# Optimization experiments

Hardware: AMD Instinct MI355X
Metric: run time of the kernel (lower is better)

Reference implementation:

```python
import jax, jax.numpy as jnp
import numpy as np
from jax import lax

B, N, K, NUM_CLASS = 8, 4096, 16, 13


def knn(pc, k):
    # pc: (B, C, N); returns indices of k nearest neighbors (B, N, k)
    sq = jnp.sum(pc * pc, axis=1)                       # (B, N)
    inner = jnp.einsum('bcn,bcm->bnm', pc, pc)          # (B, N, N)
    neg_dist = 2.0 * inner - sq[:, :, None] - sq[:, None, :]
    return lax.top_k(neg_dist, k)[1]                    # (B, N, k)


def group(fea, idx):
    # fea: (B, C, N), idx: (B, N, k) -> (B, C, N, k)
    return jax.vmap(lambda f, i: f[:, i])(fea, idx)


def mlp2(x, w, b, act=True):
    # 1x1 conv2d: x (B, Cin, N, k) -> (B, Cout, N, k)
    y = jnp.einsum('oc,bcnk->bonk', w, x) + b[None, :, None, None]
    return jax.nn.relu(y) if act else y


def mlp1(x, w, b, act=True):
    # 1x1 conv1d: x (B, Cin, N) -> (B, Cout, N)
    y = jnp.einsum('oc,bcn->bon', w, x) + b[None, :, None]
    return jax.nn.relu(y) if act else y


def edgeconv(xyz, fea, k, wg1, bg1, wg2, bg2, wf1, bf1, wf2, bf2, wf3, bf3):
    idx = knn(fea, k)
    # geometric branch: (B, 10, N, k) = [dist, xyz, xyz_knn, xyz - xyz_knn]
    xk = group(xyz, idx)
    xc = jnp.broadcast_to(xyz[:, :, :, None], xk.shape)
    xr = xc - xk
    xd = jnp.sqrt(jnp.sum(xr * xr, axis=1, keepdims=True))
    g = jnp.concatenate([xd, xc, xk, xr], axis=1)
    # feature branch: (B, 2C, N, k) = [fea, fea_knn]
    fk = group(fea, idx)
    fc = jnp.broadcast_to(fea[:, :, :, None], fk.shape)
    f = jnp.concatenate([fc, fk], axis=1)
    g = mlp2(mlp2(g, wg1, bg1), wg2, bg2)
    f = mlp2(mlp2(mlp2(f, wf1, bf1), wf2, bf2), wf3, bf3)
    return jnp.max(g * f, axis=-1)  # (B, Cout, N)


_SPECS = [
    ('e1_mg1', 10, 32), ('e1_mg2', 32, 32),
    ('e1_mf1', 6, 32), ('e1_mf2', 32, 32), ('e1_mf3', 32, 32),
    ('e2_mg1', 10, 128), ('e2_mg2', 128, 128),
    ('e2_mf1', 64, 128), ('e2_mf2', 128, 128), ('e2_mf3', 128, 128),
    ('c1', 128, 128), ('c2', 128, 1024), ('c3', 1184, 512),
    ('c4', 512, 256), ('c5', 256, 128), ('c6', 128, NUM_CLASS),
]


def setup_inputs() -> dict:
    key = jax.random.key(0)
    ks = jax.random.split(key, 2 * len(_SPECS) + 1)
    inp = {'xyz': jax.random.normal(ks[0], (B, N, 3), dtype=jnp.float32)}
    for j, (name, ci, co) in enumerate(_SPECS):
        scale = 1.0 / np.sqrt(ci)
        inp['w_' + name] = jax.random.normal(ks[2 * j + 1], (co, ci), dtype=jnp.float32) * scale
        inp['b_' + name] = jax.random.normal(ks[2 * j + 2], (co,), dtype=jnp.float32) * 0.01
    return inp


def reference(xyz, w_e1_mg1, b_e1_mg1, w_e1_mg2, b_e1_mg2, w_e1_mf1, b_e1_mf1,
              w_e1_mf2, b_e1_mf2, w_e1_mf3, b_e1_mf3, w_e2_mg1, b_e2_mg1,
              w_e2_mg2, b_e2_mg2, w_e2_mf1, b_e2_mf1, w_e2_mf2, b_e2_mf2,
              w_e2_mf3, b_e2_mf3, w_c1, b_c1, w_c2, b_c2, w_c3, b_c3,
              w_c4, b_c4, w_c5, b_c5, w_c6, b_c6):
    x = jnp.transpose(xyz, (0, 2, 1))  # (B, 3, N)
    fea1 = edgeconv(x, x, K, w_e1_mg1, b_e1_mg1, w_e1_mg2, b_e1_mg2,
                    w_e1_mf1, b_e1_mf1, w_e1_mf2, b_e1_mf2, w_e1_mf3, b_e1_mf3)
    fea2 = edgeconv(x, fea1, K, w_e2_mg1, b_e2_mg1, w_e2_mg2, b_e2_mg2,
                    w_e2_mf1, b_e2_mf1, w_e2_mf2, b_e2_mf2, w_e2_mf3, b_e2_mf3)
    f = mlp1(fea2, w_c1, b_c1)
    f = mlp1(f, w_c2, b_c2)                        # (B, 1024, N)
    g = jnp.max(f, axis=-1, keepdims=True)         # global feature (B, 1024, 1)
    g = jnp.broadcast_to(g, (g.shape[0], g.shape[1], x.shape[2]))
    f = jnp.concatenate([fea1, fea2, g], axis=1)   # (B, 1184, N)
    f = mlp1(f, w_c3, b_c3)
    f = mlp1(f, w_c4, b_c4)
    f = mlp1(f, w_c5, b_c5)
    return mlp1(f, w_c6, b_c6, act=False)          # (B, NUM_CLASS, N)
```

## Files before the change

kernel.cpp:

```cpp
#include <hip/hip_runtime.h>
#include <math.h>

#define B_ 8
#define N_ 4096

__device__ __forceinline__ unsigned short bf16rne(float x) {
    unsigned int u = __float_as_uint(x);
    return (unsigned short)((u + 0x7FFFu + ((u >> 16) & 1u)) >> 16);
}
__device__ __forceinline__ float bff(unsigned short h) {
    return __uint_as_float((unsigned int)h << 16);
}
__device__ __forceinline__ void cvt_hl(unsigned short* base, int numel, int idx, float x) {
    unsigned short h = bf16rne(x);
    base[idx] = h;
    base[numel + idx] = bf16rne(x - bff(h));
}

typedef __attribute__((ext_vector_type(8))) short bf16x8;
typedef __attribute__((ext_vector_type(4))) float f32x4;

__global__ __launch_bounds__(256) void prep_kernel(
    const float* __restrict__ w0, const float* __restrict__ w1,
    const float* __restrict__ w2, const float* __restrict__ w3,
    const float* __restrict__ w4, const float* __restrict__ w5,
    const float* __restrict__ w6, const float* __restrict__ w8,
    const float* __restrict__ w9, const float* __restrict__ w10,
    const float* __restrict__ w11, const float* __restrict__ w12,
    const float* __restrict__ w13, const float* __restrict__ w14,
    const float* __restrict__ wf1, const float* __restrict__ bf1,
    const float* __restrict__ xyz,
    float* __restrict__ wt, float* __restrict__ gbuf, float* __restrict__ sqbuf) {
    const int g = blockIdx.x * 256 + threadIdx.x;
    unsigned short* wus = (unsigned short*)(wt + 3840);

    if (g < 3584) {
        if (g < 320)       { int i = g >> 5, o = g & 31;             wt[g] = w0[o * 10 + i]; }
        else if (g < 1344) { int l = g - 320;  int i = l >> 5, o = l & 31; wt[g] = w1[o * 32 + i]; }
        else if (g < 1536) { int l = g - 1344; int i = l >> 5, o = l & 31; wt[g] = w2[o * 6 + i]; }
        else if (g < 2560) { int l = g - 1536; int i = l >> 5, o = l & 31; wt[g] = w3[o * 32 + i]; }
        else               { int l = g - 2560; int i = l >> 5, o = l & 31; wt[g] = w4[o * 32 + i]; }
    }
    else if (g < 3840)   { int l = g - 3584; wt[g] = (l < 128) ? bf1[l] : 0.0f; }
    else if (g < 12032)  { int l = g - 3840; int o = l >> 5, i = l & 31;
                           float x = (o < 128) ? wf1[o * 64 + i] : wf1[(o - 128) * 64 + 32 + i];
                           cvt_hl(wus + 0, 8192, l, x); }
    else if (g < 28416)  { int l = g - 12032;  cvt_hl(wus + 16384, 16384, l, w10[l]); }
    else if (g < 159488) { int l = g - 28416;  cvt_hl(wus + 49152, 131072, l, w11[l]); }
    else if (g < 241408) { int l = g - 159488; int o = l / 160, i = l - o * 160;
                           cvt_hl(wus + 311296, 81920, l, w12[o * 1184 + i]); }
    else if (g < 372480) { int l = g - 241408; cvt_hl(wus + 475136, 131072, l, w13[l]); }
    else if (g < 405248) { int l = g - 372480; cvt_hl(wus + 737280, 32768, l, w14[l]); }
    else if (g < 409344) { int l = g - 405248; int o = l >> 5, k = l & 31;
                           float x = (k < 10) ? w5[o * 10 + k] : 0.0f;
                           cvt_hl(wus + 802816, 4096, l, x); }
    else if (g < 425728) { int l = g - 409344; cvt_hl(wus + 811008, 16384, l, w6[l]); }
    else if (g < 442112) { int l = g - 425728; cvt_hl(wus + 843776, 16384, l, w8[l]); }
    else if (g < 458496) { int l = g - 442112; cvt_hl(wus + 876544, 16384, l, w9[l]); }
    else if (g < 466688) { gbuf[g - 458496] = 0.0f; }
    else if (g < 499456) { int l = g - 466688;
                           const float* p = xyz + (size_t)l * 3;
                           sqbuf[l] = fmaf(p[0], p[0], fmaf(p[1], p[1], p[2] * p[2])); }
}

template<int C>
__global__ void sq_kernel(const float* __restrict__ F, float* __restrict__ SQ) {
    int idx = blockIdx.x * 256 + threadIdx.x;
    const float* p = F + (size_t)idx * C;
    float s = 0.0f;
    #pragma unroll
    for (int c = 0; c < C; ++c) s = fmaf(p[c], p[c], s);
    SQ[idx] = s;
}


__device__ __forceinline__ void cas_asc(unsigned long long& x, unsigned long long& y) {
    unsigned long long a = x, b = y;
    bool sw = a > b;
    x = sw ? b : a;
    y = sw ? a : b;
}

__device__ __forceinline__ void merge_top(unsigned long long (&k)[16],
                                          const unsigned long long (&o)[16]) {
    #pragma unroll
    for (int i = 0; i < 16; ++i) {
        unsigned long long bb = o[15 - i];
        if (bb > k[i]) k[i] = bb;
    }
    #pragma unroll
    for (int st = 8; st >= 1; st >>= 1)
        #pragma unroll
        for (int i = 0; i < 16; ++i)
            if ((i & st) == 0) cas_asc(k[i], k[i + st]);
}

__device__ __forceinline__ void casf(float& x, float& y, int& xi, int& yi) {
    bool sw = x > y;
    float a = sw ? y : x;  float b = sw ? x : y;
    int ai = sw ? yi : xi; int bi = sw ? xi : yi;
    x = a; y = b; xi = ai; yi = bi;
}

__device__ __forceinline__ void sort16f(float (&v)[16], int (&ix)[16]) {
    #pragma unroll
    for (int sz = 2; sz <= 16; sz <<= 1)
        #pragma unroll
        for (int st = sz >> 1; st >= 1; st >>= 1)
            #pragma unroll
            for (int i = 0; i < 16; ++i)
                if ((i & st) == 0) {
                    if ((i & sz) == 0) casf(v[i], v[i + st], ix[i], ix[i + st]);
                    else                casf(v[i + st], v[i], ix[i + st], ix[i]);
                }
}

__device__ __forceinline__ void merge_topf(float (&kv)[16], int (&ki)[16],
                                           const float (&nv)[16], const int (&ni)[16]) {
    #pragma unroll
    for (int i = 0; i < 16; ++i) {
        bool tk = nv[15 - i] > kv[i];
        kv[i] = tk ? nv[15 - i] : kv[i];
        ki[i] = tk ? ni[15 - i] : ki[i];
    }
    #pragma unroll
    for (int st = 8; st >= 1; st >>= 1)
        #pragma unroll
        for (int i = 0; i < 16; ++i)
            if ((i & st) == 0) casf(kv[i], kv[i + st], ki[i], ki[i + st]);
}

template<int C>
__global__ __launch_bounds__(256, 3) void knn_kernel(
    const float* __restrict__ F, const float* __restrict__ SQ,
    unsigned long long* __restrict__ Kout) {
    constexpr int P1F = 2 * C * 68 + 64 * 72;
    constexpr int P1W = (P1F + 1) / 2;
    constexpr int SMW = (P1W > 64 * 65) ? P1W : 64 * 65;
    __shared__ __align__(16) unsigned long long SM[SMW];
    __shared__ float sqr[64];
    __shared__ float sqc[64];
    float* Rf = (float*)SM;
    float* Cf = Rf + C * 68;
    float* Ds = Cf + C * 68;
    const int t = threadIdx.x;
    const int b = blockIdx.y;
    const int r0 = blockIdx.x * 64;
    const int half = blockIdx.z;
    const int H0 = half * 2048;
    const int rt = (t & 15) * 4, ct = (t >> 4) * 4;
    const int sr = t & 63, sq = t >> 6;

    for (int idx = t; idx < 64 * C; idx += 256) {
        int rr = idx / C, c = idx - rr * C;
        Rf[c * 68 + rr] = F[((size_t)b * N_ + r0 + rr) * C + c];
    }
    if (t < 64) sqr[t] = SQ[(size_t)b * N_ + r0 + t];

    float kv[16]; int ki[16];
    #pragma unroll
    for (int j = 0; j < 16; ++j) { kv[j] = -3.4e38f; ki[j] = 0; }

    for (int c0 = H0; c0 < H0 + 2048; c0 += 64) {
        for (int idx = t; idx < 64 * C; idx += 256) {
            int cc = idx / C, c = idx - cc * C;
            Cf[c * 68 + cc] = F[((size_t)b * N_ + c0 + cc) * C + c];
        }
        if (t < 64) sqc[t] = SQ[(size_t)b * N_ + c0 + t];
        __syncthreads();

        float acc[4][4];
        #pragma unroll
        for (int ii = 0; ii < 4; ++ii)
            #pragma unroll
            for (int jj = 0; jj < 4; ++jj) acc[ii][jj] = 0.0f;
        #pragma unroll
        for (int i = 0; i < C; ++i) {
            float a4[4], w4[4];
            *(float4*)a4 = *(const float4*)&Rf[i * 68 + rt];
            *(float4*)w4 = *(const float4*)&Cf[i * 68 + ct];
            #pragma unroll
            for (int ii = 0; ii < 4; ++ii)
                #pragma unroll
                for (int jj = 0; jj < 4; ++jj)
                    acc[ii][jj] = fmaf(a4[ii], w4[jj], acc[ii][jj]);
        }
        #pragma unroll
        for (int ii = 0; ii < 4; ++ii) {
            float e[4];
            #pragma unroll
            for (int jj = 0; jj < 4; ++jj)
                e[jj] = 2.0f * acc[ii][jj] - sqr[rt + ii] - sqc[ct + jj];
            *(float2*)&Ds[(rt + ii) * 72 + ct] = make_float2(e[0], e[1]);
            *(float2*)&Ds[(rt + ii) * 72 + ct + 2] = make_float2(e[2], e[3]);
        }
        __syncthreads();

        float nv[16]; int ni[16];
        *(float4*)&nv[0]  = *(const float4*)&Ds[sr * 72 + sq * 16 + 0];
        *(float4*)&nv[4]  = *(const float4*)&Ds[sr * 72 + sq * 16 + 4];
        *(float4*)&nv[8]  = *(const float4*)&Ds[sr * 72 + sq * 16 + 8];
        *(float4*)&nv[12] = *(const float4*)&Ds[sr * 72 + sq * 16 + 12];
        #pragma unroll
        for (int s = 0; s < 16; ++s) ni[s] = c0 + sq * 16 + s;
        sort16f(nv, ni);
        merge_topf(kv, ki, nv, ni);
    }
    __syncthreads();
    unsigned long long kl[16];
    #pragma unroll
    for (int j = 0; j < 16; ++j) {
        unsigned int u = __float_as_uint(kv[j]);
        unsigned int ou = (u & 0x80000000u) ? ~u : (u | 0x80000000u);
        kl[j] = ((unsigned long long)ou << 32) | (unsigned int)(4095 - ki[j]);
    }
    unsigned long long* QL = SM;
    #pragma unroll
    for (int j = 0; j < 16; ++j) QL[sr * 65 + sq * 16 + j] = kl[j];
    __syncthreads();
    if (t < 64) {
        unsigned long long K[16], Tt[16];
        #pragma unroll
        for (int j = 0; j < 16; ++j) K[j] = QL[t * 65 + j];
        #pragma unroll
        for (int q = 1; q < 4; ++q) {
            #pragma unroll
            for (int j = 0; j < 16; ++j) Tt[j] = QL[t * 65 + q * 16 + j];
            merge_top(K, Tt);
        }
        size_t obase = (((size_t)b * 2 + half) * N_ + r0 + t) * 16;
        #pragma unroll
        for (int j = 0; j < 16; ++j) Kout[obase + j] = K[j];
    }
}

__global__ __launch_bounds__(256) void knn_merge_kernel(
    const unsigned long long* __restrict__ Kbuf, int* __restrict__ IDX) {
    int gid = blockIdx.x * 256 + threadIdx.x;
    int b = gid >> 12, r = gid & 4095;
    unsigned long long K0[16], K1[16];
    const unsigned long long* p0 = Kbuf + (((size_t)b * 2 + 0) * N_ + r) * 16;
    const unsigned long long* p1 = Kbuf + (((size_t)b * 2 + 1) * N_ + r) * 16;
    #pragma unroll
    for (int j = 0; j < 16; ++j) { K0[j] = p0[j]; K1[j] = p1[j]; }
    merge_top(K0, K1);
    size_t ob = ((size_t)b * N_ + r) * 16;
    #pragma unroll
    for (int j = 0; j < 16; ++j)
        IDX[ob + j] = 4095 - (int)(unsigned int)(K0[15 - j] & 0xFFFFFFFFu);
}


__global__ __launch_bounds__(256, 4) void e1_kernel(
    const float* __restrict__ xyz, const int* __restrict__ idx1,
    const float* __restrict__ wte1,
    const float* __restrict__ bg1, const float* __restrict__ bg2,
    const float* __restrict__ bf1, const float* __restrict__ bf2,
    const float* __restrict__ bf3,
    float* __restrict__ fea1) {
    __shared__ __align__(16) float Ain[10 * 132];
    __shared__ __align__(16) float Bu0[32 * 132];
    __shared__ __align__(16) float Bu1[32 * 132];
    __shared__ __align__(16) float wl[3584];
    __shared__ float bl[5][32];
    __shared__ __align__(16) float Pm1[4][8][32];
    __shared__ int idxl[128];
    const int t = threadIdx.x;
    const int b = blockIdx.x >> 9;
    const int n0 = (blockIdx.x & 511) << 3;
    const int et = (t & 31) << 2;
    const int ct = (t >> 5) << 2;

    for (int i = t; i < 3584; i += 256) wl[i] = wte1[i];
    if (t < 32) {
        bl[0][t] = bg1[t]; bl[1][t] = bg2[t]; bl[2][t] = bf1[t];
        bl[3][t] = bf2[t]; bl[4][t] = bf3[t];
    }
    if (t < 128) idxl[t] = idx1[((size_t)b * N_ + n0 + (t >> 4)) * 16 + (t & 15)];
    __syncthreads();
    if (t < 128) {
        int p = t >> 4, n = n0 + p, m = idxl[t];
        const float* xc = xyz + ((size_t)b * N_ + n) * 3;
        const float* xk = xyz + ((size_t)b * N_ + m) * 3;
        float c0 = xc[0], c1v = xc[1], c2v = xc[2];
        float k0 = xk[0], k1 = xk[1], k2 = xk[2];
        float r0 = c0 - k0, r1 = c1v - k1, r2 = c2v - k2;
        Ain[0 * 132 + t] = sqrtf(r0 * r0 + r1 * r1 + r2 * r2);
        Ain[1 * 132 + t] = c0;  Ain[2 * 132 + t] = c1v; Ain[3 * 132 + t] = c2v;
        Ain[4 * 132 + t] = k0;  Ain[5 * 132 + t] = k1;  Ain[6 * 132 + t] = k2;
        Ain[7 * 132 + t] = r0;  Ain[8 * 132 + t] = r1;  Ain[9 * 132 + t] = r2;
    }
    __syncthreads();

    float acc[4][4];
    auto gem = [&](int KK, const float* Asrc, int woff) {
        #pragma unroll
        for (int ii = 0; ii < 4; ++ii)
            #pragma unroll
            for (int jj = 0; jj < 4; ++jj) acc[ii][jj] = 0.0f;
        for (int i = 0; i < KK; ++i) {
            float a4[4], w4[4];
            *(float4*)a4 = *(const float4*)&Asrc[i * 132 + et];
            *(float4*)w4 = *(const float4*)&wl[woff + i * 32 + ct];
            #pragma unroll
            for (int ii = 0; ii < 4; ++ii)
                #pragma unroll
                for (int jj = 0; jj < 4; ++jj)
                    acc[ii][jj] = fmaf(a4[ii], w4[jj], acc[ii][jj]);
        }
    };
    auto wrout = [&](float* dst, const float* brow) {
        #pragma unroll
        for (int jj = 0; jj < 4; ++jj) {
            float tmp[4];
            #pragma unroll
            for (int ii = 0; ii < 4; ++ii) tmp[ii] = fmaxf(acc[ii][jj] + brow[ct + jj], 0.0f);
            *(float4*)&dst[(ct + jj) * 132 + et] = *(float4*)tmp;
        }
    };

    gem(10, Ain, 0);          wrout(Bu1, bl[0]);   __syncthreads();
    gem(32, Bu1, 320);
    float g2r[4][4];
    #pragma unroll
    for (int ii = 0; ii < 4; ++ii)
        #pragma unroll
        for (int jj = 0; jj < 4; ++jj)
            g2r[ii][jj] = fmaxf(acc[ii][jj] + bl[1][ct + jj], 0.0f);
    gem(6, Ain + 132, 1344);  wrout(Bu0, bl[2]);   __syncthreads();
    gem(32, Bu0, 1536);       wrout(Bu1, bl[3]);   __syncthreads();
    gem(32, Bu1, 2560);

    float pm[4];
    #pragma unroll
    for (int jj = 0; jj < 4; ++jj) {
        float mx = 0.0f;
        #pragma unroll
        for (int ii = 0; ii < 4; ++ii) {
            float f3 = fmaxf(acc[ii][jj] + bl[4][ct + jj], 0.0f);
            mx = fmaxf(mx, g2r[ii][jj] * f3);
        }
        pm[jj] = mx;
    }
    const int sub = t & 3, pl = (t & 31) >> 2;
    *(float4*)&Pm1[sub][pl][ct] = *(float4*)pm;
    __syncthreads();
    {
        int p = t >> 5, c = t & 31;
        float v = fmaxf(fmaxf(Pm1[0][p][c], Pm1[1][p][c]), fmaxf(Pm1[2][p][c], Pm1[3][p][c]));
        fea1[((size_t)b * N_ + n0 + p) * 32 + c] = v;
    }
}


__global__ __launch_bounds__(256, 2) void e2_kernel(
    const float* __restrict__ xyz, const int* __restrict__ idx2,
    const float* __restrict__ CfPf,
    const unsigned short* __restrict__ wg1p, const unsigned short* __restrict__ wg2p,
    const unsigned short* __restrict__ wf2p, const unsigned short* __restrict__ wf3p,
    const float* __restrict__ bg1, const float* __restrict__ bg2,
    const float* __restrict__ bf2, const float* __restrict__ bf3,
    float* __restrict__ fea2) {
    __shared__ __align__(16) unsigned short Ah[128 * 128];
    __shared__ __align__(16) unsigned short Al[128 * 128];
    __shared__ float bb[4][128];
    __shared__ int idxl[128];
    const int t = threadIdx.x;
    const int b = blockIdx.x >> 9;
    const int n0 = (blockIdx.x & 511) << 3;
    const int lane = t & 63, w = t >> 6;
    const int wr = (w >> 1) << 6;
    const int wc = (w & 1) << 6;
    const int lr = lane & 15, lg = lane >> 4;
    const int kb = lg << 3;

    auto swz = [](int e, int bo) { return e * 256 + (bo ^ ((e & 7) << 4)); };

    for (int i = t; i < 512; i += 256) {
        const float* bp = (i < 128) ? bg1 : (i < 256) ? bg2 : (i < 384) ? bf2 : bf3;
        bb[i >> 7][i & 127] = bp[i & 127];
    }
    if (t < 128) idxl[t] = idx2[((size_t)b * N_ + n0 + (t >> 4)) * 16 + (t & 15)];
    __syncthreads();

    f32x4 acc[4][4];
    const f32x4 zz = {0.0f, 0.0f, 0.0f, 0.0f};
    auto zacc = [&]() {
        #pragma unroll
        for (int i = 0; i < 4; ++i)
            #pragma unroll
            for (int j = 0; j < 4; ++j) acc[i][j] = zz;
    };

    {
        bf16x8 gbh[4], gbl[4];
        #pragma unroll
        for (int j = 0; j < 4; ++j) {
            float gv[8];
            #pragma unroll
            for (int q = 0; q < 8; ++q) gv[q] = 0.0f;
            if (lg < 2) {
                int e = wc + j * 16 + lr;
                int p = e >> 4, m = idxl[e];
                const float* xc = xyz + ((size_t)b * N_ + n0 + p) * 3;
                const float* xk = xyz + ((size_t)b * N_ + m) * 3;
                float c0 = xc[0], c1 = xc[1], c2 = xc[2];
                float k0 = xk[0], k1 = xk[1], k2 = xk[2];
                float r0 = c0 - k0, r1 = c1 - k1, r2 = c2 - k2;
                if (lg == 0) {
                    gv[0] = sqrtf(r0 * r0 + r1 * r1 + r2 * r2);
                    gv[1] = c0; gv[2] = c1; gv[3] = c2;
                    gv[4] = k0; gv[5] = k1; gv[6] = k2; gv[7] = r0;
                } else { gv[0] = r1; gv[1] = r2; }
            }
            bf16x8 vh, vl;
            #pragma unroll
            for (int q = 0; q < 8; ++q) {
                unsigned short h = bf16rne(gv[q]);
                vh[q] = (short)h;
                vl[q] = (short)bf16rne(gv[q] - bff(h));
            }
            gbh[j] = vh; gbl[j] = vl;
        }
        zacc();
        #pragma unroll
        for (int i = 0; i < 4; ++i) {
            size_t off = (size_t)(wr + i * 16 + lr) * 32 + kb;
            bf16x8 wh = *(const bf16x8*)(wg1p + off);
            bf16x8 wl_ = *(const bf16x8*)(wg1p + 4096 + off);
            #pragma unroll
            for (int j = 0; j < 4; ++j) {
                acc[i][j] = __builtin_amdgcn_mfma_f32_16x16x32_bf16(wh, gbh[j], acc[i][j], 0, 0, 0);
                acc[i][j] = __builtin_amdgcn_mfma_f32_16x16x32_bf16(wl_, gbh[j], acc[i][j], 0, 0, 0);
                acc[i][j] = __builtin_amdgcn_mfma_f32_16x16x32_bf16(wh, gbl[j], acc[i][j], 0, 0, 0);
            }
        }
    }

    auto epi_store = [&](const float* brow) {
        #pragma unroll
        for (int i = 0; i < 4; ++i) {
            int o4 = wr + i * 16 + lg * 4;
            float bv[4];
            *(float4*)bv = *(const float4*)&brow[o4];
            #pragma unroll
            for (int j = 0; j < 4; ++j) {
                int e = wc + j * 16 + lr;
                unsigned short h[4], l[4];
                #pragma unroll
                for (int r = 0; r < 4; ++r) {
                    float v = fmaxf(acc[i][j][r] + bv[r], 0.0f);
                    h[r] = bf16rne(v);
                    l[r] = bf16rne(v - bff(h[r]));
                }
                int bo = swz(e, o4 * 2);
                *(ushort4*)((char*)Ah + bo) = make_ushort4(h[0], h[1], h[2], h[3]);
                *(ushort4*)((char*)Al + bo) = make_ushort4(l[0], l[1], l[2], l[3]);
            }
        }
    };
    epi_store(bb[0]);
    __syncthreads();

    auto gemmK = [&](const unsigned short* __restrict__ Wp) {
        zacc();
        #pragma unroll
        for (int ks = 0; ks < 4; ++ks) {
            bf16x8 xh[4], xl[4];
            #pragma unroll
            for (int j = 0; j < 4; ++j) {
                int e = wc + j * 16 + lr;
                int bo = swz(e, (ks * 32 + kb) * 2);
                xh[j] = *(const bf16x8*)((const char*)Ah + bo);
                xl[j] = *(const bf16x8*)((const char*)Al + bo);
            }
            #pragma unroll
            for (int i = 0; i < 4; ++i) {
                size_t off = (size_t)(wr + i * 16 + lr) * 128 + ks * 32 + kb;
                bf16x8 wh = *(const bf16x8*)(Wp + off);
                bf16x8 wl_ = *(const bf16x8*)(Wp + 16384 + off);
                #pragma unroll
                for (int j = 0; j < 4; ++j) {
                    acc[i][j] = __builtin_amdgcn_mfma_f32_16x16x32_bf16(wh, xh[j], acc[i][j], 0, 0, 0);
                    acc[i][j] = __builtin_amdgcn_mfma_f32_16x16x32_bf16(wl_, xh[j], acc[i][j], 0, 0, 0);
                    acc[i][j] = __builtin_amdgcn_mfma_f32_16x16x32_bf16(wh, xl[j], acc[i][j], 0, 0, 0);
                }
            }
        }
    };

    gemmK(wg2p);
    float g2r[4][4][4];
    #pragma unroll
    for (int i = 0; i < 4; ++i) {
        float bv[4];
        *(float4*)bv = *(const float4*)&bb[1][wr + i * 16 + lg * 4];
        #pragma unroll
        for (int j = 0; j < 4; ++j)
            #pragma unroll
            for (int r = 0; r < 4; ++r)
                g2r[i][j][r] = fmaxf(acc[i][j][r] + bv[r], 0.0f);
    }
    __syncthreads();

    {
        int e = t & 127, hf = t >> 7;
        int n = n0 + (e >> 4), m = idxl[e];
        const float* crow = CfPf + ((size_t)b * N_ + n) * 256 + hf * 64;
        const float* prow = CfPf + ((size_t)b * N_ + m) * 256 + 128 + hf * 64;
        #pragma unroll
        for (int q = 0; q < 16; ++q) {
            float4 cc = *(const float4*)(crow + q * 4);
            float4 pp = *(const float4*)(prow + q * 4);
            float v[4] = { fmaxf(cc.x + pp.x, 0.0f), fmaxf(cc.y + pp.y, 0.0f),
                           fmaxf(cc.z + pp.z, 0.0f), fmaxf(cc.w + pp.w, 0.0f) };
            unsigned short h[4], l[4];
            #pragma unroll
            for (int r = 0; r < 4; ++r) {
                h[r] = bf16rne(v[r]);
                l[r] = bf16rne(v[r] - bff(h[r]));
            }
            int bo = swz(e, (hf * 64 + q * 4) * 2);
            *(ushort4*)((char*)Ah + bo) = make_ushort4(h[0], h[1], h[2], h[3]);
            *(ushort4*)((char*)Al + bo) = make_ushort4(l[0], l[1], l[2], l[3]);
        }
    }
    __syncthreads();

    gemmK(wf2p);
    __syncthreads();
    epi_store(bb[2]);
    __syncthreads();

    gemmK(wf3p);
    #pragma unroll
    for (int j = 0; j < 4; ++j) {
        int p = (wc >> 4) + j;
        #pragma unroll
        for (int i = 0; i < 4; ++i) {
            int o4 = wr + i * 16 + lg * 4;
            float bv[4];
            *(float4*)bv = *(const float4*)&bb[3][o4];
            float vr[4];
            #pragma unroll
            for (int r = 0; r < 4; ++r) {
                float f3v = fmaxf(acc[i][j][r] + bv[r], 0.0f);
                float v = g2r[i][j][r] * f3v;
                v = fmaxf(v, __shfl_xor(v, 1));
                v = fmaxf(v, __shfl_xor(v, 2));
                v = fmaxf(v, __shfl_xor(v, 4));
                v = fmaxf(v, __shfl_xor(v, 8));
                vr[r] = v;
            }
            if (lr == 0)
                *(float4*)(fea2 + ((size_t)b * N_ + n0 + p) * 128 + o4) = *(float4*)vr;
        }
    }
}


template<int RELU, int BMODE, int GMAX>
__global__ __launch_bounds__(256) void gemm_mfma(
    const float* __restrict__ X1, int S1, int K1,
    const float* __restrict__ X2, int S2, int Ktot,
    const unsigned short* __restrict__ Wc, const float* __restrict__ bias,
    float* __restrict__ Y, int COUT, float* __restrict__ gout) {
    __shared__ __align__(16) unsigned short Xh[128 * 40];
    __shared__ __align__(16) unsigned short Xl[128 * 40];
    __shared__ __align__(16) unsigned short Wh[128 * 40];
    __shared__ __align__(16) unsigned short Wl[128 * 40];
    __shared__ float Gm[2][128];
    const int t = threadIdx.x;
    const int m0 = blockIdx.x * 128, o0 = blockIdx.y * 128;
    const int lane = t & 63, w = t >> 6;
    const int wr = (w >> 1) << 6, wc = (w & 1) << 6;
    const int lr = lane & 15, lg = lane >> 4;
    const int kb = lg << 3;
    const size_t WN = (size_t)COUT * Ktot;

    f32x4 acc[4][4];
    const f32x4 zz = {0.0f, 0.0f, 0.0f, 0.0f};
    #pragma unroll
    for (int i = 0; i < 4; ++i)
        #pragma unroll
        for (int j = 0; j < 4; ++j) acc[i][j] = zz;

    const int ntile = Ktot >> 5;
    for (int kt = 0; kt < ntile; ++kt) {
        const int kbase = kt << 5;
        const float* Xp; int S, koff;
        if (kbase < K1) { Xp = X1; S = S1; koff = kbase; }
        else            { Xp = X2; S = S2; koff = kbase - K1; }
        #pragma unroll
        for (int rr = 0; rr < 4; ++rr) {
            int idx = t + rr * 256;
            int p = idx >> 3, i4 = (idx & 7) << 2;
            const float4 v = *(const float4*)(Xp + (size_t)(m0 + p) * S + koff + i4);
            unsigned short h0 = bf16rne(v.x), h1 = bf16rne(v.y);
            unsigned short h2 = bf16rne(v.z), h3 = bf16rne(v.w);
            *(ushort4*)&Xh[p * 40 + i4] = make_ushort4(h0, h1, h2, h3);
            *(ushort4*)&Xl[p * 40 + i4] = make_ushort4(
                bf16rne(v.x - bff(h0)), bf16rne(v.y - bff(h1)),
                bf16rne(v.z - bff(h2)), bf16rne(v.w - bff(h3)));
        }
        #pragma unroll
        for (int rr = 0; rr < 2; ++rr) {
            int c = t + rr * 256;
            int o = c >> 2, k8 = (c & 3) << 3;
            const unsigned short* src = Wc + (size_t)(o0 + o) * Ktot + kbase + k8;
            *(uint4*)&Wh[o * 40 + k8] = *(const uint4*)src;
            *(uint4*)&Wl[o * 40 + k8] = *(const uint4*)(src + WN);
        }
        __syncthreads();

        bf16x8 ah[4], al[4], bh[4], bl[4];
        #pragma unroll
        for (int f = 0; f < 4; ++f) {
            ah[f] = *(const bf16x8*)&Xh[(wr + f * 16 + lr) * 40 + kb];
            al[f] = *(const bf16x8*)&Xl[(wr + f * 16 + lr) * 40 + kb];
            bh[f] = *(const bf16x8*)&Wh[(wc + f * 16 + lr) * 40 + kb];
            bl[f] = *(const bf16x8*)&Wl[(wc + f * 16 + lr) * 40 + kb];
        }
        #pragma unroll
        for (int i = 0; i < 4; ++i)
            #pragma unroll
            for (int j = 0; j < 4; ++j) {
                acc[i][j] = __builtin_amdgcn_mfma_f32_16x16x32_bf16(ah[i], bh[j], acc[i][j], 0, 0, 0);
                acc[i][j] = __builtin_amdgcn_mfma_f32_16x16x32_bf16(al[i], bh[j], acc[i][j], 0, 0, 0);
                acc[i][j] = __builtin_amdgcn_mfma_f32_16x16x32_bf16(ah[i], bl[j], acc[i][j], 0, 0, 0);
            }
        __syncthreads();
    }

    const int b = m0 >> 12;
    if (GMAX) {
        #pragma unroll
        for (int j = 0; j < 4; ++j) {
            const int oc = wc + j * 16 + lr;
            const float bv = bias[o0 + oc];
            float mx = 0.0f;
            #pragma unroll
            for (int i = 0; i < 4; ++i)
                #pragma unroll
                for (int r = 0; r < 4; ++r) {
                    float v = acc[i][j][r] + bv;
                    if (RELU) v = fmaxf(v, 0.0f);
                    mx = fmaxf(mx, v);
                }
            mx = fmaxf(mx, __shfl_xor(mx, 16));
            mx = fmaxf(mx, __shfl_xor(mx, 32));
            if (lane < 16) Gm[w >> 1][wc + j * 16 + lane] = mx;
        }
        __syncthreads();
        if (t < 128) {
            float v = fmaxf(Gm[0][t], Gm[1][t]);
            atomicMax((unsigned int*)(gout + b * 1024 + o0 + t), __float_as_uint(v));
        }
    } else {
        #pragma unroll
        for (int j = 0; j < 4; ++j) {
            const int oc = wc + j * 16 + lr;
            const float bv = (BMODE == 0) ? bias[o0 + oc] : bias[b * 512 + o0 + oc];
            #pragma unroll
            for (int i = 0; i < 4; ++i) {
                float* yp = Y + (size_t)(m0 + wr + i * 16 + lg * 4) * COUT + o0 + oc;
                #pragma unroll
                for (int r = 0; r < 4; ++r) {
                    float v = acc[i][j][r] + bv;
                    if (RELU) v = fmaxf(v, 0.0f);
                    yp[(size_t)r * COUT] = v;
                }
            }
        }
    }
}


__global__ void bias3_kernel(const float* __restrict__ g, const float* __restrict__ w_c3,
                             const float* __restrict__ b_c3, float* __restrict__ bias3) {
    __shared__ float gs[1024];
    int b = blockIdx.x >> 1;
    int o = ((blockIdx.x & 1) << 8) + threadIdx.x;
    for (int i = threadIdx.x; i < 1024; i += 256) gs[i] = g[b * 1024 + i];
    __syncthreads();
    float acc = b_c3[o];
    const float* wr = w_c3 + (size_t)o * 1184 + 160;
    for (int i = 0; i < 1024; i += 4) {
        float4 w4 = *(const float4*)(wr + i);
        acc = fmaf(w4.x, gs[i], acc);     acc = fmaf(w4.y, gs[i + 1], acc);
        acc = fmaf(w4.z, gs[i + 2], acc); acc = fmaf(w4.w, gs[i + 3], acc);
    }
    bias3[b * 512 + o] = acc;
}


__global__ __launch_bounds__(256, 1) void c6_kernel(
    const float* __restrict__ h5, const float* __restrict__ w,
    const float* __restrict__ bias, float* __restrict__ out) {
    __shared__ float ws[13 * 128];
    __shared__ float bs[13];
    int t = threadIdx.x;
    for (int i = t; i < 13 * 128; i += 256) ws[i] = w[i];
    if (t < 13) bs[t] = bias[t];
    __syncthreads();
    int b = blockIdx.x >> 4;
    int n = ((blockIdx.x & 15) << 8) + t;
    float x[128];
    const float* xp = h5 + ((size_t)b * N_ + n) * 128;
    #pragma unroll
    for (int i = 0; i < 128; i += 4) *(float4*)&x[i] = *(const float4*)(xp + i);
    for (int o = 0; o < 13; ++o) {
        float acc = bs[o];
        #pragma unroll
        for (int i = 0; i < 128; ++i) acc = fmaf(ws[o * 128 + i], x[i], acc);
        out[((size_t)b * 13 + o) * N_ + n] = acc;
    }
}


extern "C" void kernel_launch(void* const* d_in, const int* in_sizes, int n_in,
                              void* d_out, int out_size, void* d_ws, size_t ws_size,
                              hipStream_t stream) {
    (void)in_sizes; (void)n_in; (void)out_size; (void)ws_size;
    const float* xyz = (const float*)d_in[0];
    #define W_(j)  ((const float*)d_in[1 + 2 * (j)])
    #define Bp_(j) ((const float*)d_in[2 + 2 * (j)])

    char* ws = (char*)d_ws;
    const size_t MB = 1u << 20;
    int*   idx1  = (int*)(ws + 0 * MB);
    int*   idx2  = (int*)(ws + 2 * MB);
    float* fea1  = (float*)(ws + 4 * MB);
    float* CfPf  = (float*)(ws + 8 * MB);
    float* fea2  = (float*)(ws + 40 * MB);
    float* h1    = (float*)(ws + 56 * MB);
    float* sqbuf = (float*)(ws + 72 * MB);
    float* gbuf  = (float*)(ws + 72 * MB + (128u << 10));
    float* b3buf = (float*)(ws + 72 * MB + (160u << 10));
    float* wt    = (float*)(ws + 72 * MB + (176u << 10));
    float* h3    = (float*)(ws + 75 * MB);
    float* h4    = CfPf;
    float* h5    = h1;
    float* outp  = (float*)d_out;
    unsigned long long* Kbuf = (unsigned long long*)(ws + 75 * MB);

    float* wte1  = wt;
    float* bpre  = wt + 3584;
    const unsigned short* wus = (const unsigned short*)(wt + 3840);
    const unsigned short* wpre = wus + 0;
    const unsigned short* wc1  = wus + 16384;
    const unsigned short* wc2  = wus + 49152;
    const unsigned short* wc3  = wus + 311296;
    const unsigned short* wc4  = wus + 475136;
    const unsigned short* wc5  = wus + 737280;
    const unsigned short* wg1p = wus + 802816;
    const unsigned short* wg2p = wus + 811008;
    const unsigned short* wf2p = wus + 843776;
    const unsigned short* wf3p = wus + 876544;

    prep_kernel<<<1951, 256, 0, stream>>>(
        W_(0), W_(1), W_(2), W_(3), W_(4), W_(5), W_(6), W_(8), W_(9), W_(10),
        W_(11), W_(12), W_(13), W_(14), W_(7), Bp_(7), xyz, wt, gbuf, sqbuf);

    knn_kernel<3><<<dim3(64, 8, 2), 256, 0, stream>>>(xyz, sqbuf, Kbuf);
    knn_merge_kernel<<<128, 256, 0, stream>>>(Kbuf, idx1);
    e1_kernel<<<4096, 256, 0, stream>>>(xyz, idx1, wte1, Bp_(0), Bp_(1), Bp_(2), Bp_(3), Bp_(4), fea1);

    sq_kernel<32><<<128, 256, 0, stream>>>(fea1, sqbuf);
    knn_kernel<32><<<dim3(64, 8, 2), 256, 0, stream>>>(fea1, sqbuf, Kbuf);
    knn_merge_kernel<<<128, 256, 0, stream>>>(Kbuf, idx2);
    gemm_mfma<0, 0, 0><<<dim3(256, 2), 256, 0, stream>>>(fea1, 32, 32, nullptr, 0, 32,
                                                         wpre, bpre, CfPf, 256, nullptr);
    e2_kernel<<<4096, 256, 0, stream>>>(xyz, idx2, CfPf, wg1p, wg2p, wf2p, wf3p,
                                        Bp_(5), Bp_(6), Bp_(8), Bp_(9), fea2);

    gemm_mfma<1, 0, 0><<<dim3(256, 1), 256, 0, stream>>>(fea2, 128, 128, nullptr, 0, 128,
                                                         wc1, Bp_(10), h1, 128, nullptr);
    gemm_mfma<1, 0, 1><<<dim3(256, 8), 256, 0, stream>>>(h1, 128, 128, nullptr, 0, 128,
                                                         wc2, Bp_(11), nullptr, 1024, gbuf);
    bias3_kernel<<<16, 256, 0, stream>>>(gbuf, W_(12), Bp_(12), b3buf);
    gemm_mfma<1, 1, 0><<<dim3(256, 4), 256, 0, stream>>>(fea1, 32, 32, fea2, 128, 160,
                                                         wc3, b3buf, h3, 512, nullptr);
    gemm_mfma<1, 0, 0><<<dim3(256, 2), 256, 0, stream>>>(h3, 512, 512, nullptr, 0, 512,
                                                         wc4, Bp_(13), h4, 256, nullptr);
    gemm_mfma<1, 0, 0><<<dim3(256, 1), 256, 0, stream>>>(h4, 256, 256, nullptr, 0, 256,
                                                         wc5, Bp_(14), h5, 128, nullptr);
    c6_kernel<<<128, 256, 0, stream>>>(h5, W_(15), Bp_(15), outp);
    #undef W_
    #undef Bp_
}
```

Measured before the change: 1.216 ms.

## Move KNN distance computation to bf16x3 MFMA with two-pass threshold selection

The KNN kernel now computes the pairwise inner products on MFMA units, using a three-way bf16 split (high/mid/low) of the features that prep_kernel and a new fea1p_kernel pack ahead of time. It runs two passes: the first keeps only the sorted top-16 values per row to derive a threshold, and the second recomputes distances and collects candidates at or above that threshold into shared memory via atomics, then sorts them with their indices. This avoids carrying index arrays through the bitonic sorts and removes the fp32 FMA inner loop, at the cost of doing the MFMA work twice and reading operands directly from global memory. Candidate capture is capped at 32 per row, so ties could drop entries, and the split-bf16 product may not match fp32 bit-for-bit.

```diff
diff --git a/kernel.cpp b/kernel.cpp
--- a/kernel.cpp
+++ b/kernel.cpp
@@ -3,6 +3,7 @@
 
 #define B_ 8
 #define N_ 4096
+#define PL_ (8 * 4096 * 32)
 
 __device__ __forceinline__ unsigned short bf16rne(float x) {
     unsigned int u = __float_as_uint(x);
@@ -19,6 +20,8 @@
 
 typedef __attribute__((ext_vector_type(8))) short bf16x8;
 typedef __attribute__((ext_vector_type(4))) float f32x4;
+
+#define MF16(a, b, c) __builtin_amdgcn_mfma_f32_16x16x32_bf16((a), (b), (c), 0, 0, 0)
 
 __global__ __launch_bounds__(256) void prep_kernel(
     const float* __restrict__ w0, const float* __restrict__ w1,
@@ -30,7 +33,8 @@
     const float* __restrict__ w13, const float* __restrict__ w14,
     const float* __restrict__ wf1, const float* __restrict__ bf1,
     const float* __restrict__ xyz,
-    float* __restrict__ wt, float* __restrict__ gbuf, float* __restrict__ sqbuf) {
+    float* __restrict__ wt, float* __restrict__ gbuf, float* __restrict__ sqbuf,
+    unsigned short* __restrict__ xyzp) {
     const int g = blockIdx.x * 256 + threadIdx.x;
     unsigned short* wus = (unsigned short*)(wt + 3840);
 
@@ -61,16 +65,51 @@
     else if (g < 499456) { int l = g - 466688;
                            const float* p = xyz + (size_t)l * 3;
                            sqbuf[l] = fmaf(p[0], p[0], fmaf(p[1], p[1], p[2] * p[2])); }
-}
-
-template<int C>
-__global__ void sq_kernel(const float* __restrict__ F, float* __restrict__ SQ) {
-    int idx = blockIdx.x * 256 + threadIdx.x;
-    const float* p = F + (size_t)idx * C;
+    else if (g < 532224) {
+        int row = g - 499456;
+        const float* p = xyz + (size_t)row * 3;
+        unsigned short hv[8] = {0,0,0,0,0,0,0,0};
+        unsigned short mv[8] = {0,0,0,0,0,0,0,0};
+        unsigned short lv[8] = {0,0,0,0,0,0,0,0};
+        #pragma unroll
+        for (int c = 0; c < 3; ++c) {
+            float v = p[c];
+            unsigned short h = bf16rne(v); float d = v - bff(h);
+            unsigned short m = bf16rne(d);
+            hv[c] = h; mv[c] = m; lv[c] = bf16rne(d - bff(m));
+        }
+        uint4 z = make_uint4(0u, 0u, 0u, 0u);
+        unsigned short* d0 = xyzp + (size_t)row * 32;
+        unsigned short* d1 = d0 + PL_;
+        unsigned short* d2 = d0 + 2 * PL_;
+        *(uint4*)d0 = *(uint4*)hv; *(uint4*)(d0 + 8) = z; *(uint4*)(d0 + 16) = z; *(uint4*)(d0 + 24) = z;
+        *(uint4*)d1 = *(uint4*)mv; *(uint4*)(d1 + 8) = z; *(uint4*)(d1 + 16) = z; *(uint4*)(d1 + 24) = z;
+        *(uint4*)d2 = *(uint4*)lv; *(uint4*)(d2 + 8) = z; *(uint4*)(d2 + 16) = z; *(uint4*)(d2 + 24) = z;
+    }
+}
+
+__global__ __launch_bounds__(256) void fea1p_kernel(
+    const float* __restrict__ F, unsigned short* __restrict__ P, float* __restrict__ SQ) {
+    int row = blockIdx.x * 256 + threadIdx.x;
+    const float* x = F + (size_t)row * 32;
     float s = 0.0f;
-    #pragma unroll
-    for (int c = 0; c < C; ++c) s = fmaf(p[c], p[c], s);
-    SQ[idx] = s;
+    unsigned short hb[32], mb[32], lb[32];
+    #pragma unroll
+    for (int c = 0; c < 32; ++c) {
+        float v = x[c];
+        s = fmaf(v, v, s);
+        unsigned short h = bf16rne(v); float d = v - bff(h);
+        unsigned short m = bf16rne(d);
+        hb[c] = h; mb[c] = m; lb[c] = bf16rne(d - bff(m));
+    }
+    SQ[row] = s;
+    unsigned short* d0 = P + (size_t)row * 32;
+    #pragma unroll
+    for (int q = 0; q < 4; ++q) {
+        *(uint4*)(d0 + 8 * q)           = *(uint4*)&hb[8 * q];
+        *(uint4*)(d0 + PL_ + 8 * q)     = *(uint4*)&mb[8 * q];
+        *(uint4*)(d0 + 2 * PL_ + 8 * q) = *(uint4*)&lb[8 * q];
+    }
 }
 
 
@@ -95,14 +134,12 @@
             if ((i & st) == 0) cas_asc(k[i], k[i + st]);
 }
 
-__device__ __forceinline__ void casf(float& x, float& y, int& xi, int& yi) {
-    bool sw = x > y;
-    float a = sw ? y : x;  float b = sw ? x : y;
-    int ai = sw ? yi : xi; int bi = sw ? xi : yi;
-    x = a; y = b; xi = ai; yi = bi;
-}
-
-__device__ __forceinline__ void sort16f(float (&v)[16], int (&ix)[16]) {
+__device__ __forceinline__ void casv(float& x, float& y) {
+    float lo = fminf(x, y), hi = fmaxf(x, y);
+    x = lo; y = hi;
+}
+
+__device__ __forceinline__ void sortv16(float (&v)[16]) {
     #pragma unroll
     for (int sz = 2; sz <= 16; sz <<= 1)
         #pragma unroll
@@ -110,123 +147,151 @@
             #pragma unroll
             for (int i = 0; i < 16; ++i)
                 if ((i & st) == 0) {
-                    if ((i & sz) == 0) casf(v[i], v[i + st], ix[i], ix[i + st]);
-                    else                casf(v[i + st], v[i], ix[i + st], ix[i]);
+                    if ((i & sz) == 0) casv(v[i], v[i + st]);
+                    else                casv(v[i + st], v[i]);
                 }
 }
 
-__device__ __forceinline__ void merge_topf(float (&kv)[16], int (&ki)[16],
-                                           const float (&nv)[16], const int (&ni)[16]) {
-    #pragma unroll
-    for (int i = 0; i < 16; ++i) {
-        bool tk = nv[15 - i] > kv[i];
-        kv[i] = tk ? nv[15 - i] : kv[i];
-        ki[i] = tk ? ni[15 - i] : ki[i];
-    }
+__device__ __forceinline__ void mergev(float (&kv)[16], const float (&nv)[16]) {
+    #pragma unroll
+    for (int i = 0; i < 16; ++i) kv[i] = fmaxf(kv[i], nv[15 - i]);
     #pragma unroll
     for (int st = 8; st >= 1; st >>= 1)
         #pragma unroll
         for (int i = 0; i < 16; ++i)
-            if ((i & st) == 0) casf(kv[i], kv[i + st], ki[i], ki[i + st]);
-}
-
-template<int C>
-__global__ __launch_bounds__(256, 3) void knn_kernel(
-    const float* __restrict__ F, const float* __restrict__ SQ,
+            if ((i & st) == 0) casv(kv[i], kv[i + st]);
+}
+
+__global__ __launch_bounds__(256, 4) void knn_kernel(
+    const unsigned short* __restrict__ P, const float* __restrict__ SQ,
     unsigned long long* __restrict__ Kout) {
-    constexpr int P1F = 2 * C * 68 + 64 * 72;
-    constexpr int P1W = (P1F + 1) / 2;
-    constexpr int SMW = (P1W > 64 * 65) ? P1W : 64 * 65;
-    __shared__ __align__(16) unsigned long long SM[SMW];
-    __shared__ float sqr[64];
-    __shared__ float sqc[64];
-    float* Rf = (float*)SM;
-    float* Cf = Rf + C * 68;
-    float* Ds = Cf + C * 68;
+    __shared__ __align__(16) char U[64 * 68 * 4];
+    __shared__ float sqcL[2048];
+    __shared__ float tau[64];
+    __shared__ int cnt[64];
+    float* Ds = (float*)U;
+    unsigned long long* cap = (unsigned long long*)U;
     const int t = threadIdx.x;
     const int b = blockIdx.y;
     const int r0 = blockIdx.x * 64;
     const int half = blockIdx.z;
     const int H0 = half * 2048;
-    const int rt = (t & 15) * 4, ct = (t >> 4) * 4;
+    const int lane = t & 63, w = t >> 6;
+    const int lr = lane & 15, lg = lane >> 4;
+    const int kb = lg << 3;
     const int sr = t & 63, sq = t >> 6;
-
-    for (int idx = t; idx < 64 * C; idx += 256) {
-        int rr = idx / C, c = idx - rr * C;
-        Rf[c * 68 + rr] = F[((size_t)b * N_ + r0 + rr) * C + c];
-    }
-    if (t < 64) sqr[t] = SQ[(size_t)b * N_ + r0 + t];
-
-    float kv[16]; int ki[16];
-    #pragma unroll
-    for (int j = 0; j < 16; ++j) { kv[j] = -3.4e38f; ki[j] = 0; }
+    const int pw = lg ^ (w & 3);
+    const int psr = ((sr >> 2) ^ (sr >> 4)) & 3;
+
+    for (int i = t; i < 2048; i += 256) sqcL[i] = SQ[(size_t)b * N_ + H0 + i];
+
+    const unsigned short* ap = P + ((size_t)(b * N_) + r0 + 16 * w + lr) * 32 + kb;
+    const bf16x8 ah = *(const bf16x8*)ap;
+    const bf16x8 am = *(const bf16x8*)(ap + PL_);
+    const bf16x8 al = *(const bf16x8*)(ap + 2 * PL_);
+    const f32x4 sqr4 = *(const f32x4*)&SQ[(size_t)b * N_ + r0 + 16 * w + 4 * lg];
+
+    float kv[16];
+    #pragma unroll
+    for (int j = 0; j < 16; ++j) kv[j] = -3.4e38f;
+
+    __syncthreads();
 
     for (int c0 = H0; c0 < H0 + 2048; c0 += 64) {
-        for (int idx = t; idx < 64 * C; idx += 256) {
-            int cc = idx / C, c = idx - cc * C;
-            Cf[c * 68 + cc] = F[((size_t)b * N_ + c0 + cc) * C + c];
-        }
-        if (t < 64) sqc[t] = SQ[(size_t)b * N_ + c0 + t];
+        #pragma unroll
+        for (int j = 0; j < 4; ++j) {
+            const unsigned short* bp = P + ((size_t)(b * N_) + c0 + 16 * j + lr) * 32 + kb;
+            bf16x8 bh = *(const bf16x8*)bp;
+            bf16x8 bm = *(const bf16x8*)(bp + PL_);
+            bf16x8 bl = *(const bf16x8*)(bp + 2 * PL_);
+            f32x4 a = {0.0f, 0.0f, 0.0f, 0.0f};
+            a = MF16(ah, bh, a); a = MF16(am, bh, a); a = MF16(ah, bm, a);
+            a = MF16(am, bm, a); a = MF16(al, bh, a); a = MF16(ah, bl, a);
+            float sqcv = sqcL[c0 - H0 + 16 * j + lr];
+            int colsw = 16 * j + ((((lr >> 2) ^ pw) & 3) << 2) + (lr & 3);
+            #pragma unroll
+            for (int r = 0; r < 4; ++r) {
+                float e = fmaf(2.0f, a[r], -sqr4[r]) - sqcv;
+                Ds[(16 * w + 4 * lg + r) * 68 + colsw] = e;
+            }
+        }
         __syncthreads();
-
-        float acc[4][4];
-        #pragma unroll
-        for (int ii = 0; ii < 4; ++ii)
-            #pragma unroll
-            for (int jj = 0; jj < 4; ++jj) acc[ii][jj] = 0.0f;
-        #pragma unroll
-        for (int i = 0; i < C; ++i) {
-            float a4[4], w4[4];
-            *(float4*)a4 = *(const float4*)&Rf[i * 68 + rt];
-            *(float4*)w4 = *(const float4*)&Cf[i * 68 + ct];
-            #pragma unroll
-            for (int ii = 0; ii < 4; ++ii)
+        float nv[16];
+        #pragma unroll
+        for (int q = 0; q < 4; ++q)
+            *(float4*)&nv[4 * q] = *(const float4*)&Ds[sr * 68 + sq * 16 + (((q ^ psr) & 3) << 2)];
+        sortv16(nv);
+        mergev(kv, nv);
+        __syncthreads();
+    }
+
+    float* QLf = (float*)U;
+    #pragma unroll
+    for (int j = 0; j < 16; ++j) QLf[sr * 68 + sq * 16 + j] = kv[j];
+    __syncthreads();
+    if (t < 64) {
+        float K[16];
+        #pragma unroll
+        for (int j = 0; j < 16; ++j) K[j] = QLf[t * 68 + j];
+        #pragma unroll
+        for (int q = 1; q < 4; ++q) {
+            float Tt[16];
+            #pragma unroll
+            for (int j = 0; j < 16; ++j) Tt[j] = QLf[t * 68 + q * 16 + j];
+            #pragma unroll
+            for (int i = 0; i < 16; ++i) K[i] = fmaxf(K[i], Tt[15 - i]);
+            #pragma unroll
+            for (int st = 8; st >= 1; st >>= 1)
                 #pragma unroll
-                for (int jj = 0; jj < 4; ++jj)
-                    acc[ii][jj] = fmaf(a4[ii], w4[jj], acc[ii][jj]);
-        }
-        #pragma unroll
-        for (int ii = 0; ii < 4; ++ii) {
-            float e[4];
-            #pragma unroll
-            for (int jj = 0; jj < 4; ++jj)
-                e[jj] = 2.0f * acc[ii][jj] - sqr[rt + ii] - sqc[ct + jj];
-            *(float2*)&Ds[(rt + ii) * 72 + ct] = make_float2(e[0], e[1]);
-            *(float2*)&Ds[(rt + ii) * 72 + ct + 2] = make_float2(e[2], e[3]);
-        }
-        __syncthreads();
-
-        float nv[16]; int ni[16];
-        *(float4*)&nv[0]  = *(const float4*)&Ds[sr * 72 + sq * 16 + 0];
-        *(float4*)&nv[4]  = *(const float4*)&Ds[sr * 72 + sq * 16 + 4];
-        *(float4*)&nv[8]  = *(const float4*)&Ds[sr * 72 + sq * 16 + 8];
-        *(float4*)&nv[12] = *(const float4*)&Ds[sr * 72 + sq * 16 + 12];
-        #pragma unroll
-        for (int s = 0; s < 16; ++s) ni[s] = c0 + sq * 16 + s;
-        sort16f(nv, ni);
-        merge_topf(kv, ki, nv, ni);
-    }
-    __syncthreads();
-    unsigned long long kl[16];
-    #pragma unroll
-    for (int j = 0; j < 16; ++j) {
-        unsigned int u = __float_as_uint(kv[j]);
-        unsigned int ou = (u & 0x80000000u) ? ~u : (u | 0x80000000u);
-        kl[j] = ((unsigned long long)ou << 32) | (unsigned int)(4095 - ki[j]);
-    }
-    unsigned long long* QL = SM;
-    #pragma unroll
-    for (int j = 0; j < 16; ++j) QL[sr * 65 + sq * 16 + j] = kl[j];
-    __syncthreads();
+                for (int i = 0; i < 16; ++i)
+                    if ((i & st) == 0) casv(K[i], K[i + st]);
+        }
+        tau[t] = K[0];
+        cnt[t] = 0;
+    }
+    __syncthreads();
+    const f32x4 taur4 = *(const f32x4*)&tau[16 * w + 4 * lg];
+
+    for (int c0 = H0; c0 < H0 + 2048; c0 += 64) {
+        #pragma unroll
+        for (int j = 0; j < 4; ++j) {
+            const unsigned short* bp = P + ((size_t)(b * N_) + c0 + 16 * j + lr) * 32 + kb;
+            bf16x8 bh = *(const bf16x8*)bp;
+            bf16x8 bm = *(const bf16x8*)(bp + PL_);
+            bf16x8 bl = *(const bf16x8*)(bp + 2 * PL_);
+            f32x4 a = {0.0f, 0.0f, 0.0f, 0.0f};
+            a = MF16(ah, bh, a); a = MF16(am, bh, a); a = MF16(ah, bm, a);
+            a = MF16(am, bm, a); a = MF16(al, bh, a); a = MF16(ah, bl, a);
+            float sqcv = sqcL[c0 - H0 + 16 * j + lr];
+            #pragma unroll
+            for (int r = 0; r < 4; ++r) {
+                float e = fmaf(2.0f, a[r], -sqr4[r]) - sqcv;
+                if (e >= taur4[r]) {
+                    int row = 16 * w + 4 * lg + r;
+                    unsigned int u = __float_as_uint(e);
+                    unsigned int ou = (u & 0x80000000u) ? ~u : (u | 0x80000000u);
+                    unsigned long long key = ((unsigned long long)ou << 32)
+                                           | (unsigned int)(4095 - (c0 + 16 * j + lr));
+                    int pos = atomicAdd(&cnt[row], 1);
+                    if (pos < 32) cap[row * 32 + pos] = key;
+                }
+            }
+        }
+    }
+    __syncthreads();
+
     if (t < 64) {
-        unsigned long long K[16], Tt[16];
-        #pragma unroll
-        for (int j = 0; j < 16; ++j) K[j] = QL[t * 65 + j];
-        #pragma unroll
-        for (int q = 1; q < 4; ++q) {
-            #pragma unroll
-            for (int j = 0; j < 16; ++j) Tt[j] = QL[t * 65 + q * 16 + j];
-            merge_top(K, Tt);
+        int n = min(cnt[t], 32);
+        unsigned long long K[16];
+        #pragma unroll
+        for (int j = 0; j < 16; ++j) K[j] = 0ull;
+        for (int i = 0; i < n; ++i) {
+            unsigned long long v = cap[t * 32 + i];
+            if (v > K[0]) {
+                K[0] = v;
+                #pragma unroll
+                for (int s = 0; s < 15; ++s) cas_asc(K[s], K[s + 1]);
+            }
         }
         size_t obase = (((size_t)b * 2 + half) * N_ + r0 + t) * 16;
         #pragma unroll
@@ -430,9 +495,9 @@
             bf16x8 wl_ = *(const bf16x8*)(wg1p + 4096 + off);
             #pragma unroll
             for (int j = 0; j < 4; ++j) {
-                acc[i][j] = __builtin_amdgcn_mfma_f32_16x16x32_bf16(wh, gbh[j], acc[i][j], 0, 0, 0);
-                acc[i][j] = __builtin_amdgcn_mfma_f32_16x16x32_bf16(wl_, gbh[j], acc[i][j], 0, 0, 0);
-                acc[i][j] = __builtin_amdgcn_mfma_f32_16x16x32_bf16(wh, gbl[j], acc[i][j], 0, 0, 0);
+                acc[i][j] = MF16(wh, gbh[j], acc[i][j]);
+                acc[i][j] = MF16(wl_, gbh[j], acc[i][j]);
+                acc[i][j] = MF16(wh, gbl[j], acc[i][j]);
             }
         }
     }
@@ -481,9 +546,9 @@
                 bf16x8 wl_ = *(const bf16x8*)(Wp + 16384 + off);
                 #pragma unroll
                 for (int j = 0; j < 4; ++j) {
-                    acc[i][j] = __builtin_amdgcn_mfma_f32_16x16x32_bf16(wh, xh[j], acc[i][j], 0, 0, 0);
-                    acc[i][j] = __builtin_amdgcn_mfma_f32_16x16x32_bf16(wl_, xh[j], acc[i][j], 0, 0, 0);
-                    acc[i][j] = __builtin_amdgcn_mfma_f32_16x16x32_bf16(wh, xl[j], acc[i][j], 0, 0, 0);
+                    acc[i][j] = MF16(wh, xh[j], acc[i][j]);
+                    acc[i][j] = MF16(wl_, xh[j], acc[i][j]);
+                    acc[i][j] = MF16(wh, xl[j], acc[i][j]);
                 }
             }
         }
@@ -625,9 +690,9 @@
         for (int i = 0; i < 4; ++i)
             #pragma unroll
             for (int j = 0; j < 4; ++j) {
-                acc[i][j] = __builtin_amdgcn_mfma_f32_16x16x32_bf16(ah[i], bh[j], acc[i][j], 0, 0, 0);
-                acc[i][j] = __builtin_amdgcn_mfma_f32_16x16x32_bf16(al[i], bh[j], acc[i][j], 0, 0, 0);
-                acc[i][j] = __builtin_amdgcn_mfma_f32_16x16x32_bf16(ah[i], bl[j], acc[i][j], 0, 0, 0);
+                acc[i][j] = MF16(ah[i], bh[j], acc[i][j]);
+                acc[i][j] = MF16(al[i], bh[j], acc[i][j]);
+                acc[i][j] = MF16(ah[i], bl[j], acc[i][j]);
             }
         __syncthreads();
     }
@@ -743,6 +808,8 @@
     float* h5    = h1;
     float* outp  = (float*)d_out;
     unsigned long long* Kbuf = (unsigned long long*)(ws + 75 * MB);
+    unsigned short* xyzp = (unsigned short*)(ws + 8 * MB);
+    unsigned short* feap = (unsigned short*)(ws + 14 * MB);
 
     float* wte1  = wt;
     float* bpre  = wt + 3584;
@@ -758,16 +825,16 @@
     const unsigned short* wf2p = wus + 843776;
     const unsigned short* wf3p = wus + 876544;
 
-    prep_kernel<<<1951, 256, 0, stream>>>(
+    prep_kernel<<<2079, 256, 0, stream>>>(
         W_(0), W_(1), W_(2), W_(3), W_(4), W_(5), W_(6), W_(8), W_(9), W_(10),
-        W_(11), W_(12), W_(13), W_(14), W_(7), Bp_(7), xyz, wt, gbuf, sqbuf);
-
-    knn_kernel<3><<<dim3(64, 8, 2), 256, 0, stream>>>(xyz, sqbuf, Kbuf);
+        W_(11), W_(12), W_(13), W_(14), W_(7), Bp_(7), xyz, wt, gbuf, sqbuf, xyzp);
+
+    knn_kernel<<<dim3(64, 8, 2), 256, 0, stream>>>(xyzp, sqbuf, Kbuf);
     knn_merge_kernel<<<128, 256, 0, stream>>>(Kbuf, idx1);
     e1_kernel<<<4096, 256, 0, stream>>>(xyz, idx1, wte1, Bp_(0), Bp_(1), Bp_(2), Bp_(3), Bp_(4), fea1);
 
-    sq_kernel<32><<<128, 256, 0, stream>>>(fea1, sqbuf);
-    knn_kernel<32><<<dim3(64, 8, 2), 256, 0, stream>>>(fea1, sqbuf, Kbuf);
+    fea1p_kernel<<<128, 256, 0, stream>>>(fea1, feap, sqbuf);
+    knn_kernel<<<dim3(64, 8, 2), 256, 0, stream>>>(feap, sqbuf, Kbuf);
     knn_merge_kernel<<<128, 256, 0, stream>>>(Kbuf, idx2);
     gemm_mfma<0, 0, 0><<<dim3(256, 2), 256, 0, stream>>>(fea1, 32, 32, nullptr, 0, 32,
                                                          wpre, bpre, CfPf, 256, nullptr);
```

Result: faster. 1.162 ms (-4.4%).
